# Optimization experiments

Hardware: AMD Instinct MI355X
Metric: run time of the kernel (lower is better)

The kernel has to match this reference:

```python
import jax, jax.numpy as jnp
import numpy as np

GI_DIM = 1220
HID = 150
GIJ = 3 * GI_DIM + 60  # 3720


def setup_inputs() -> dict:
    key = jax.random.key(0)
    ks = jax.random.split(key, 16)
    N, P = 50000, 100000
    inp = {
        "g_i": jax.random.normal(ks[0], (N, GI_DIM), jnp.float32),
        "mention_scores": jax.random.normal(ks[1], (N,), jnp.float32),
        "dist_emb": jax.random.normal(ks[2], (9, 20), jnp.float32) * 0.1,
        "genre_emb": jax.random.normal(ks[3], (8, 20), jnp.float32) * 0.1,
        "speaker_emb": jax.random.normal(ks[4], (3, 20), jnp.float32) * 0.1,
        "W1": jax.random.normal(ks[5], (GIJ, HID), jnp.float32) / np.sqrt(GIJ),
        "b1": jnp.zeros((HID,), jnp.float32),
        "W2": jax.random.normal(ks[6], (HID, HID), jnp.float32) / np.sqrt(HID),
        "b2": jnp.zeros((HID,), jnp.float32),
        "W3": jax.random.normal(ks[7], (HID, 1), jnp.float32) / np.sqrt(HID),
        "b3": jnp.zeros((1,), jnp.float32),
        "mention_ids": jax.random.randint(ks[8], (P,), 0, N, jnp.int64 if jax.config.jax_enable_x64 else jnp.int32),
        "antecedent_ids": jax.random.randint(ks[9], (P,), 0, N, jnp.int32),
        "distance_ids": jax.random.randint(ks[10], (P,), 0, 9, jnp.int32),
        "genre_ids": jax.random.randint(ks[11], (P,), 0, 8, jnp.int32),
        "speaker_ids": jax.random.randint(ks[12], (P,), 0, 3, jnp.int32),
    }
    return inp


def reference(g_i, mention_scores, dist_emb, genre_emb, speaker_emb,
              W1, b1, W2, b2, W3, b3,
              mention_ids, antecedent_ids, distance_ids, genre_ids, speaker_ids):
    # phi: [P, 60] pair features (distance, genre, speaker embeddings)
    phi = jnp.concatenate([dist_emb[distance_ids],
                           genre_emb[genre_ids],
                           speaker_emb[speaker_ids]], axis=1)
    i_g = g_i[mention_ids]      # [P, GI_DIM]
    j_g = g_i[antecedent_ids]   # [P, GI_DIM]
    pairs = jnp.concatenate([i_g, j_g, i_g * j_g, phi], axis=1)  # [P, GIJ]
    h = jax.nn.relu(pairs @ W1 + b1)
    h = jax.nn.relu(h @ W2 + b2)
    pairwise = (h @ W3 + b3)[:, 0]  # [P]
    sij = mention_scores[mention_ids] + mention_scores[antecedent_ids] + pairwise
    return sij
```

## Files before the change

kernel.cpp:

```cpp
#include <hip/hip_runtime.h>

#define GI  1220
#define KP  1280
#define BK  128
#define NCH (KP / BK)
#define NP  192
#define ABW 320

typedef __bf16        bf16x8 __attribute__((ext_vector_type(8)));
typedef float         f32x4  __attribute__((ext_vector_type(4)));
typedef unsigned int  u32x4  __attribute__((ext_vector_type(4)));
typedef unsigned int  u32x2  __attribute__((ext_vector_type(2)));

__device__ __forceinline__ unsigned short f2bf(float f) {
  __bf16 h = (__bf16)f;
  return __builtin_bit_cast(unsigned short, h);
}
__device__ __forceinline__ float bf2f(unsigned short u) {
  return (float)__builtin_bit_cast(__bf16, u);
}
__device__ __forceinline__ unsigned int pk2(float a, float b) {
  return (unsigned int)f2bf(a) | ((unsigned int)f2bf(b) << 16);
}
__device__ __forceinline__ unsigned int mulbf2(unsigned int a, unsigned int b) {
  float xl = __builtin_bit_cast(float, a << 16);
  float xh = __builtin_bit_cast(float, a & 0xffff0000u);
  float yl = __builtin_bit_cast(float, b << 16);
  float yh = __builtin_bit_cast(float, b & 0xffff0000u);
  return pk2(xl * yl, xh * yh);
}

__global__ void prep_kernel(const float* __restrict__ W1, const float* __restrict__ W2,
                            const float* __restrict__ b1,
                            const float* __restrict__ de, const float* __restrict__ ge,
                            const float* __restrict__ se,
                            unsigned short* __restrict__ W1ab_t,
                            unsigned short* __restrict__ W1c_t,
                            unsigned short* __restrict__ W2_t,
                            float* __restrict__ projs) {
  int idx = blockIdx.x * 256 + threadIdx.x;
  const int R1 = ABW * KP, R2 = NP * KP, R3 = NP * NP, R4 = 20 * NP;
  if (idx < R1) {
    int n = idx / KP, k = idx % KP;
    float v = 0.f;
    if (k < GI) {
      if (n < 150)                 v = W1[k * 150 + n];
      else if (n >= 160 && n < 310) v = W1[(GI + k) * 150 + (n - 160)];
    }
    W1ab_t[idx] = f2bf(v);
    return;
  }
  idx -= R1;
  if (idx < R2) {
    int n = idx / KP, k = idx % KP;
    float v = (k < GI && n < 150) ? W1[(2 * GI + k) * 150 + n] : 0.f;
    W1c_t[idx] = f2bf(v);
    return;
  }
  idx -= R2;
  if (idx < R3) {
    int n = idx / NP, k = idx % NP;
    float v = (n < 150 && k < 150) ? W2[k * 150 + n] : 0.f;
    W2_t[idx] = f2bf(v);
    return;
  }
  idx -= R3;
  if (idx < R4) {
    int r = idx / NP, n = idx % NP;
    float v = 0.f;
    if (n < 150) {
      if (r < 9) {
        v = b1[n];
        for (int t = 0; t < 20; ++t) v += de[r * 20 + t] * W1[(3660 + t) * 150 + n];
      } else if (r < 17) {
        int q = r - 9;
        for (int t = 0; t < 20; ++t) v += ge[q * 20 + t] * W1[(3680 + t) * 150 + n];
      } else {
        int q = r - 17;
        for (int t = 0; t < 20; ++t) v += se[q * 20 + t] * W1[(3700 + t) * 150 + n];
      }
    }
    projs[idx] = v;
  }
}

__global__ __launch_bounds__(256, 3)
void ab_kernel(const float* __restrict__ g, const unsigned short* __restrict__ W1ab_t,
               unsigned short* __restrict__ AB, unsigned short* __restrict__ gpad,
               int N) {
  __shared__ __attribute__((aligned(16))) unsigned short sX[64 * 136];
  const int t = threadIdx.x;
  const int m0 = blockIdx.x * 64;
  const int w = t >> 6, lane = t & 63, quad = lane >> 4, lm = lane & 15;

  f32x4 acc[4][5];
#pragma unroll
  for (int a = 0; a < 4; ++a)
#pragma unroll
    for (int b = 0; b < 5; ++b) { acc[a][b].x = 0.f; acc[a][b].y = 0.f; acc[a][b].z = 0.f; acc[a][b].w = 0.f; }

  const int r = t >> 2, s = t & 3;
  int row = m0 + r; if (row >= N) row = N - 1;
  const float* gr = g + (long)row * GI;

  for (int c = 0; c < NCH; ++c) {
    __syncthreads();
#pragma unroll
    for (int i = 0; i < 8; ++i) {
      int k = c * BK + i * 16 + s * 4;
      u32x2 pk; pk.x = 0u; pk.y = 0u;
      if (k < GI) {
        f32x4 x = *(const f32x4*)(gr + k);
        pk.x = pk2(x.x, x.y);
        pk.y = pk2(x.z, x.w);
      }
      *(u32x2*)&sX[r * 136 + i * 16 + s * 4] = pk;
      if (gpad) *(u32x2*)(gpad + (long)row * KP + k) = pk;
    }
    __syncthreads();
#pragma unroll
    for (int kk = 0; kk < 4; ++kk) {
      bf16x8 af[4];
#pragma unroll
      for (int mi = 0; mi < 4; ++mi)
        af[mi] = __builtin_bit_cast(bf16x8, *(const u32x4*)&sX[(mi * 16 + lm) * 136 + kk * 32 + quad * 8]);
#pragma unroll
      for (int tl = 0; tl < 5; ++tl) {
        int n = (w * 5 + tl) * 16 + lm;
        bf16x8 bfr = __builtin_bit_cast(bf16x8, *(const u32x4*)(W1ab_t + n * KP + c * BK + kk * 32 + quad * 8));
#pragma unroll
        for (int mi = 0; mi < 4; ++mi)
          acc[mi][tl] = __builtin_amdgcn_mfma_f32_16x16x32_bf16(af[mi], bfr, acc[mi][tl], 0, 0, 0);
      }
    }
  }
#pragma unroll
  for (int mi = 0; mi < 4; ++mi)
#pragma unroll
    for (int reg = 0; reg < 4; ++reg) {
      int m = m0 + mi * 16 + quad * 4 + reg;
      if (m < N) {
#pragma unroll
        for (int tl = 0; tl < 5; ++tl) {
          int n = (w * 5 + tl) * 16 + lm;
          AB[(long)m * ABW + n] = f2bf(acc[mi][tl][reg]);
        }
      }
    }
}

template <bool PADG>
__global__ __launch_bounds__(256, 5)
void pair_kernel(const float* __restrict__ g, const unsigned short* __restrict__ gpad,
                 const float* __restrict__ msc,
                 const unsigned short* __restrict__ AB,
                 const unsigned short* __restrict__ W1c_t,
                 const unsigned short* __restrict__ W2_t,
                 const float* __restrict__ projs,
                 const float* __restrict__ b2, const float* __restrict__ W3,
                 const float* __restrict__ b3,
                 const int* __restrict__ mid, const int* __restrict__ aid,
                 const int* __restrict__ did, const int* __restrict__ gid,
                 const int* __restrict__ sid,
                 float* __restrict__ out, int P) {
  __shared__ __attribute__((aligned(16))) unsigned short sX[64 * 200];
  __shared__ int sM[64], sA[64], sDGS[64];

  const int t = threadIdx.x;
  const int p0 = blockIdx.x * 64;
  const int w = t >> 6, lane = t & 63, quad = lane >> 4, lm = lane & 15;

  if (t < 64) {
    int p = p0 + t;
    int m_ = 0, a_ = 0, dgs = 0;
    if (p < P) {
      m_ = mid[p]; a_ = aid[p];
      dgs = did[p] | (gid[p] << 4) | (sid[p] << 8);
    }
    sM[t] = m_; sA[t] = a_; sDGS[t] = dgs;
  }
  __syncthreads();

  const int r = t >> 2, s = t & 3;

  f32x4 acc[4][3];
#pragma unroll
  for (int a = 0; a < 4; ++a)
#pragma unroll
    for (int b = 0; b < 3; ++b) { acc[a][b].x = 0.f; acc[a][b].y = 0.f; acc[a][b].z = 0.f; acc[a][b].w = 0.f; }

  const float* gm32; const float* ga32;
  const unsigned short* gm16; const unsigned short* ga16;
  if constexpr (PADG) {
    gm16 = gpad + (long)sM[r] * KP;
    ga16 = gpad + (long)sA[r] * KP;
  } else {
    gm32 = g + (long)sM[r] * GI;
    ga32 = g + (long)sA[r] * GI;
  }

  for (int c = 0; c < NCH; ++c) {
    __syncthreads();
    if constexpr (PADG) {
#pragma unroll
      for (int i = 0; i < 4; ++i) {
        int k = c * BK + i * 32 + s * 8;
        u32x4 xx = *(const u32x4*)(gm16 + k);
        u32x4 yy = *(const u32x4*)(ga16 + k);
        u32x4 o;
        o.x = mulbf2(xx.x, yy.x);
        o.y = mulbf2(xx.y, yy.y);
        o.z = mulbf2(xx.z, yy.z);
        o.w = mulbf2(xx.w, yy.w);
        *(u32x4*)&sX[r * 136 + i * 32 + s * 8] = o;
      }
    } else {
#pragma unroll
      for (int i = 0; i < 8; ++i) {
        int k = c * BK + i * 16 + s * 4;
        u32x2 pk; pk.x = 0u; pk.y = 0u;
        if (k < GI) {
          f32x4 x = *(const f32x4*)(gm32 + k);
          f32x4 y = *(const f32x4*)(ga32 + k);
          pk.x = pk2(x.x * y.x, x.y * y.y);
          pk.y = pk2(x.z * y.z, x.w * y.w);
        }
        *(u32x2*)&sX[r * 136 + i * 16 + s * 4] = pk;
      }
    }
    __syncthreads();
#pragma unroll
    for (int kk = 0; kk < 4; ++kk) {
      bf16x8 af[4];
#pragma unroll
      for (int mi = 0; mi < 4; ++mi)
        af[mi] = __builtin_bit_cast(bf16x8, *(const u32x4*)&sX[(mi * 16 + lm) * 136 + kk * 32 + quad * 8]);
#pragma unroll
      for (int tl = 0; tl < 3; ++tl) {
        int n = (w * 3 + tl) * 16 + lm;
        bf16x8 bfr = __builtin_bit_cast(bf16x8, *(const u32x4*)(W1c_t + n * KP + c * BK + kk * 32 + quad * 8));
#pragma unroll
        for (int mi = 0; mi < 4; ++mi)
          acc[mi][tl] = __builtin_amdgcn_mfma_f32_16x16x32_bf16(af[mi], bfr, acc[mi][tl], 0, 0, 0);
      }
    }
  }
  __syncthreads();

  {
    const unsigned short* Ar = AB + (long)sM[r] * ABW;
    const unsigned short* Br = AB + (long)sA[r] * ABW + 160;
    int dgs = sDGS[r];
    const float* dp = projs + (dgs & 15) * NP;
    const float* gp = projs + (9 + ((dgs >> 4) & 15)) * NP;
    const float* sp = projs + (17 + (dgs >> 8)) * NP;
#pragma unroll
    for (int j = 0; j < 6; ++j) {
      int n = s * 48 + j * 8;
      f32x4 p0v = *(const f32x4*)(dp + n) + *(const f32x4*)(gp + n) + *(const f32x4*)(sp + n);
      f32x4 p1v = *(const f32x4*)(dp + n + 4) + *(const f32x4*)(gp + n + 4) + *(const f32x4*)(sp + n + 4);
      if (n < 160) {
        u32x4 a8 = *(const u32x4*)(Ar + n);
        u32x4 b8 = *(const u32x4*)(Br + n);
        p0v.x += bf2f(a8.x & 0xffff) + bf2f(b8.x & 0xffff);
        p0v.y += bf2f(a8.x >> 16)    + bf2f(b8.x >> 16);
        p0v.z += bf2f(a8.y & 0xffff) + bf2f(b8.y & 0xffff);
        p0v.w += bf2f(a8.y >> 16)    + bf2f(b8.y >> 16);
        p1v.x += bf2f(a8.z & 0xffff) + bf2f(b8.z & 0xffff);
        p1v.y += bf2f(a8.z >> 16)    + bf2f(b8.z >> 16);
        p1v.z += bf2f(a8.w & 0xffff) + bf2f(b8.w & 0xffff);
        p1v.w += bf2f(a8.w >> 16)    + bf2f(b8.w >> 16);
      }
      u32x4 o;
      o.x = pk2(p0v.x, p0v.y); o.y = pk2(p0v.z, p0v.w);
      o.z = pk2(p1v.x, p1v.y); o.w = pk2(p1v.z, p1v.w);
      *(u32x4*)&sX[r * 200 + n] = o;
    }
  }
  __syncthreads();

#pragma unroll
  for (int mi = 0; mi < 4; ++mi)
#pragma unroll
    for (int tl = 0; tl < 3; ++tl) {
      int n = (w * 3 + tl) * 16 + lm;
#pragma unroll
      for (int reg = 0; reg < 4; ++reg) {
        int m = mi * 16 + quad * 4 + reg;
        float v = acc[mi][tl][reg] + bf2f(sX[m * 200 + n]);
        sX[m * 200 + n] = f2bf(fmaxf(v, 0.f));
      }
    }
  __syncthreads();

  f32x4 acc2[4][3];
#pragma unroll
  for (int a = 0; a < 4; ++a)
#pragma unroll
    for (int b = 0; b < 3; ++b) { acc2[a][b].x = 0.f; acc2[a][b].y = 0.f; acc2[a][b].z = 0.f; acc2[a][b].w = 0.f; }
#pragma unroll
  for (int kk = 0; kk < 6; ++kk) {
    bf16x8 af[4];
#pragma unroll
    for (int mi = 0; mi < 4; ++mi)
      af[mi] = __builtin_bit_cast(bf16x8, *(const u32x4*)&sX[(mi * 16 + lm) * 200 + kk * 32 + quad * 8]);
#pragma unroll
    for (int tl = 0; tl < 3; ++tl) {
      int n = (w * 3 + tl) * 16 + lm;
      bf16x8 bfr = __builtin_bit_cast(bf16x8, *(const u32x4*)(W2_t + n * NP + kk * 32 + quad * 8));
#pragma unroll
      for (int mi = 0; mi < 4; ++mi)
        acc2[mi][tl] = __builtin_amdgcn_mfma_f32_16x16x32_bf16(af[mi], bfr, acc2[mi][tl], 0, 0, 0);
    }
  }
  __syncthreads();

#pragma unroll
  for (int mi = 0; mi < 4; ++mi)
#pragma unroll
    for (int tl = 0; tl < 3; ++tl) {
      int n = (w * 3 + tl) * 16 + lm;
      float bb = (n < 150) ? b2[n] : 0.f;
#pragma unroll
      for (int reg = 0; reg < 4; ++reg) {
        int m = mi * 16 + quad * 4 + reg;
        float v = acc2[mi][tl][reg] + bb;
        sX[m * 200 + n] = f2bf(fmaxf(v, 0.f));
      }
    }
  __syncthreads();

  {
    float sum = 0.f;
#pragma unroll
    for (int j = 0; j < 48; ++j) {
      int n = s * 48 + j;
      if (n < 150) sum += bf2f(sX[r * 200 + n]) * W3[n];
    }
    sum += __shfl_xor(sum, 1);
    sum += __shfl_xor(sum, 2);
    if (s == 0) {
      int p = p0 + r;
      if (p < P) out[p] = msc[sM[r]] + msc[sA[r]] + sum + b3[0];
    }
  }
}

extern "C" void kernel_launch(void* const* d_in, const int* in_sizes, int n_in,
                              void* d_out, int out_size, void* d_ws, size_t ws_size,
                              hipStream_t stream) {
  (void)n_in; (void)out_size;
  const float* g   = (const float*)d_in[0];
  const float* msc = (const float*)d_in[1];
  const float* de  = (const float*)d_in[2];
  const float* ge  = (const float*)d_in[3];
  const float* se  = (const float*)d_in[4];
  const float* W1  = (const float*)d_in[5];
  const float* b1  = (const float*)d_in[6];
  const float* W2  = (const float*)d_in[7];
  const float* b2  = (const float*)d_in[8];
  const float* W3  = (const float*)d_in[9];
  const float* b3  = (const float*)d_in[10];
  const int* mid = (const int*)d_in[11];
  const int* aid = (const int*)d_in[12];
  const int* did = (const int*)d_in[13];
  const int* gid = (const int*)d_in[14];
  const int* sid = (const int*)d_in[15];
  const int N = in_sizes[0] / GI;
  const int P = in_sizes[11];
  float* out = (float*)d_out;

  char* ws = (char*)d_ws;
  size_t off = 0;
  auto alloc = [&](size_t bytes) { char* p = ws + off; off = (off + bytes + 255) & ~(size_t)255; return p; };
  unsigned short* AB     = (unsigned short*)alloc((size_t)N * ABW * 2);
  unsigned short* W1ab_t = (unsigned short*)alloc((size_t)ABW * KP * 2);
  unsigned short* W1c_t  = (unsigned short*)alloc((size_t)NP * KP * 2);
  unsigned short* W2_t   = (unsigned short*)alloc((size_t)NP * NP * 2);
  float* projs           = (float*)alloc((size_t)20 * NP * 4);

  size_t gpad_bytes = (size_t)N * KP * 2;
  unsigned short* gpad = nullptr;
  if (off + gpad_bytes + 256 <= ws_size)
    gpad = (unsigned short*)alloc(gpad_bytes);

  const int prep_total = ABW * KP + NP * KP + NP * NP + 20 * NP;
  prep_kernel<<<(prep_total + 255) / 256, 256, 0, stream>>>(W1, W2, b1, de, ge, se,
                                                            W1ab_t, W1c_t, W2_t, projs);
  ab_kernel<<<(N + 63) / 64, 256, 0, stream>>>(g, W1ab_t, AB, gpad, N);
  if (gpad)
    pair_kernel<true><<<(P + 63) / 64, 256, 0, stream>>>(g, gpad, msc, AB, W1c_t, W2_t, projs,
                                                         b2, W3, b3, mid, aid, did, gid, sid, out, P);
  else
    pair_kernel<false><<<(P + 63) / 64, 256, 0, stream>>>(g, gpad, msc, AB, W1c_t, W2_t, projs,
                                                          b2, W3, b3, mid, aid, did, gid, sid, out, P);
}
```

Baseline: 831.0 us.

## Per-wave pair tiles with register prefetch, split bf16 conversion, double-buffered AB GEMM

Restructures the pair kernel so each wave owns its own 16 pairs and all 192 output columns. This removes block-wide __syncthreads and prefetches the next chunk of gathered rows into registers while the MFMAs run. The fp32-to-bf16 conversion of g moves into a separate convert kernel. The AB GEMM now double-buffers its LDS tile with an XOR swizzle and prefetches from the bf16 copy. The trade-offs are more registers per wave (occupancy hint lowered from 5 to 4), and each wave now reads the whole of W1c_t itself instead of sharing it across the block.

```diff
diff --git a/kernel.cpp b/kernel.cpp
--- a/kernel.cpp
+++ b/kernel.cpp
@@ -10,7 +10,6 @@
 typedef __bf16        bf16x8 __attribute__((ext_vector_type(8)));
 typedef float         f32x4  __attribute__((ext_vector_type(4)));
 typedef unsigned int  u32x4  __attribute__((ext_vector_type(4)));
-typedef unsigned int  u32x2  __attribute__((ext_vector_type(2)));
 
 __device__ __forceinline__ unsigned short f2bf(float f) {
   __bf16 h = (__bf16)f;
@@ -44,7 +43,7 @@
     int n = idx / KP, k = idx % KP;
     float v = 0.f;
     if (k < GI) {
-      if (n < 150)                 v = W1[k * 150 + n];
+      if (n < 150)                  v = W1[k * 150 + n];
       else if (n >= 160 && n < 310) v = W1[(GI + k) * 150 + (n - 160)];
     }
     W1ab_t[idx] = f2bf(v);
@@ -84,14 +83,31 @@
   }
 }
 
+__global__ __launch_bounds__(256)
+void convert_kernel(const float* __restrict__ g, unsigned short* __restrict__ gpad, int N) {
+  int idx = blockIdx.x * 256 + threadIdx.x;
+  int total = N * (KP / 8);
+  if (idx >= total) return;
+  int row = idx / (KP / 8);
+  int u   = idx - row * (KP / 8);
+  int k0  = u * 8;
+  u32x4 o; o.x = 0u; o.y = 0u; o.z = 0u; o.w = 0u;
+  const float* gr = g + (long)row * GI;
+  if (k0 + 4 <= GI) { f32x4 a = *(const f32x4*)(gr + k0);     o.x = pk2(a.x, a.y); o.y = pk2(a.z, a.w); }
+  if (k0 + 8 <= GI) { f32x4 b = *(const f32x4*)(gr + k0 + 4); o.z = pk2(b.x, b.y); o.w = pk2(b.z, b.w); }
+  *(u32x4*)(gpad + (long)row * KP + k0) = o;
+}
+
+template <bool PADG>
 __global__ __launch_bounds__(256, 3)
-void ab_kernel(const float* __restrict__ g, const unsigned short* __restrict__ W1ab_t,
-               unsigned short* __restrict__ AB, unsigned short* __restrict__ gpad,
-               int N) {
-  __shared__ __attribute__((aligned(16))) unsigned short sX[64 * 136];
+void ab_kernel(const float* __restrict__ g, const unsigned short* __restrict__ gpad,
+               const unsigned short* __restrict__ W1ab_t,
+               unsigned short* __restrict__ AB, int N) {
+  __shared__ __attribute__((aligned(16))) unsigned short sX[2][8192];
   const int t = threadIdx.x;
   const int m0 = blockIdx.x * 64;
   const int w = t >> 6, lane = t & 63, quad = lane >> 4, lm = lane & 15;
+  const int cb = (t & 15) ^ (t >> 4);
 
   f32x4 acc[4][5];
 #pragma unroll
@@ -99,35 +115,44 @@
 #pragma unroll
     for (int b = 0; b < 5; ++b) { acc[a][b].x = 0.f; acc[a][b].y = 0.f; acc[a][b].z = 0.f; acc[a][b].w = 0.f; }
 
-  const int r = t >> 2, s = t & 3;
-  int row = m0 + r; if (row >= N) row = N - 1;
-  const float* gr = g + (long)row * GI;
-
+  u32x4 stg[4];
+  auto fetch = [&](int c, u32x4 st[4]) {
+#pragma unroll
+    for (int j = 0; j < 4; ++j) {
+      int row = m0 + j * 16 + (t >> 4); if (row >= N) row = N - 1;
+      int k = c * BK + cb * 8;
+      if constexpr (PADG) {
+        st[j] = *(const u32x4*)(gpad + (long)row * KP + k);
+      } else {
+        u32x4 o; o.x = 0u; o.y = 0u; o.z = 0u; o.w = 0u;
+        const float* gr = g + (long)row * GI + k;
+        if (k + 4 <= GI) { f32x4 a = *(const f32x4*)gr;       o.x = pk2(a.x, a.y); o.y = pk2(a.z, a.w); }
+        if (k + 8 <= GI) { f32x4 b = *(const f32x4*)(gr + 4); o.z = pk2(b.x, b.y); o.w = pk2(b.z, b.w); }
+        st[j] = o;
+      }
+    }
+  };
+
+  fetch(0, stg);
   for (int c = 0; c < NCH; ++c) {
-    __syncthreads();
-#pragma unroll
-    for (int i = 0; i < 8; ++i) {
-      int k = c * BK + i * 16 + s * 4;
-      u32x2 pk; pk.x = 0u; pk.y = 0u;
-      if (k < GI) {
-        f32x4 x = *(const f32x4*)(gr + k);
-        pk.x = pk2(x.x, x.y);
-        pk.y = pk2(x.z, x.w);
-      }
-      *(u32x2*)&sX[r * 136 + i * 16 + s * 4] = pk;
-      if (gpad) *(u32x2*)(gpad + (long)row * KP + k) = pk;
-    }
+    unsigned short* buf = sX[c & 1];
+#pragma unroll
+    for (int j = 0; j < 4; ++j)
+      *(u32x4*)(buf + (j * 256 + t) * 8) = stg[j];
+    if (c + 1 < NCH) fetch(c + 1, stg);
     __syncthreads();
 #pragma unroll
     for (int kk = 0; kk < 4; ++kk) {
       bf16x8 af[4];
 #pragma unroll
-      for (int mi = 0; mi < 4; ++mi)
-        af[mi] = __builtin_bit_cast(bf16x8, *(const u32x4*)&sX[(mi * 16 + lm) * 136 + kk * 32 + quad * 8]);
+      for (int mi = 0; mi < 4; ++mi) {
+        int row = mi * 16 + lm;
+        af[mi] = __builtin_bit_cast(bf16x8, *(const u32x4*)(buf + row * 128 + (((kk * 4 + quad) ^ lm) * 8)));
+      }
 #pragma unroll
       for (int tl = 0; tl < 5; ++tl) {
         int n = (w * 5 + tl) * 16 + lm;
-        bf16x8 bfr = __builtin_bit_cast(bf16x8, *(const u32x4*)(W1ab_t + n * KP + c * BK + kk * 32 + quad * 8));
+        bf16x8 bfr = __builtin_bit_cast(bf16x8, *(const u32x4*)(W1ab_t + (long)n * KP + c * BK + kk * 32 + quad * 8));
 #pragma unroll
         for (int mi = 0; mi < 4; ++mi)
           acc[mi][tl] = __builtin_amdgcn_mfma_f32_16x16x32_bf16(af[mi], bfr, acc[mi][tl], 0, 0, 0);
@@ -150,7 +175,7 @@
 }
 
 template <bool PADG>
-__global__ __launch_bounds__(256, 5)
+__global__ __launch_bounds__(256, 4)
 void pair_kernel(const float* __restrict__ g, const unsigned short* __restrict__ gpad,
                  const float* __restrict__ msc,
                  const unsigned short* __restrict__ AB,
@@ -163,103 +188,120 @@
                  const int* __restrict__ did, const int* __restrict__ gid,
                  const int* __restrict__ sid,
                  float* __restrict__ out, int P) {
-  __shared__ __attribute__((aligned(16))) unsigned short sX[64 * 200];
-  __shared__ int sM[64], sA[64], sDGS[64];
-
+  __shared__ __attribute__((aligned(16))) unsigned short sW[4][16 * 200];
   const int t = threadIdx.x;
-  const int p0 = blockIdx.x * 64;
   const int w = t >> 6, lane = t & 63, quad = lane >> 4, lm = lane & 15;
-
-  if (t < 64) {
-    int p = p0 + t;
-    int m_ = 0, a_ = 0, dgs = 0;
-    if (p < P) {
-      m_ = mid[p]; a_ = aid[p];
-      dgs = did[p] | (gid[p] << 4) | (sid[p] << 8);
-    }
-    sM[t] = m_; sA[t] = a_; sDGS[t] = dgs;
-  }
-  __syncthreads();
-
-  const int r = t >> 2, s = t & 3;
-
-  f32x4 acc[4][3];
-#pragma unroll
-  for (int a = 0; a < 4; ++a)
-#pragma unroll
-    for (int b = 0; b < 3; ++b) { acc[a][b].x = 0.f; acc[a][b].y = 0.f; acc[a][b].z = 0.f; acc[a][b].w = 0.f; }
-
-  const float* gm32; const float* ga32;
-  const unsigned short* gm16; const unsigned short* ga16;
+  unsigned short* sWw = sW[w];
+
+  const int pw0 = blockIdx.x * 64 + w * 16;
+
+  int mv = 0, av = 0, dv = 0;
+  float scv = 0.f;
+  if (lane < 16) {
+    int p = pw0 + lane; if (p >= P) p = P - 1;
+    mv = mid[p]; av = aid[p];
+    dv = did[p] | (gid[p] << 4) | (sid[p] << 8);
+    scv = msc[mv] + msc[av];
+  }
+  const int mi_ = __shfl(mv, lm);
+  const int ai_ = __shfl(av, lm);
+  const int dgs = __shfl(dv, lm);
+
+  const int rr = lane & 15;
+  const int colq = lane >> 4;
+
+  f32x4 acc[12];
+#pragma unroll
+  for (int i = 0; i < 12; ++i) { acc[i].x = 0.f; acc[i].y = 0.f; acc[i].z = 0.f; acc[i].w = 0.f; }
+
   if constexpr (PADG) {
-    gm16 = gpad + (long)sM[r] * KP;
-    ga16 = gpad + (long)sA[r] * KP;
+    const unsigned short* gmr = gpad + (long)mi_ * KP;
+    const unsigned short* gar = gpad + (long)ai_ * KP;
+    u32x4 xr[2], yr[2];
+    auto fetch = [&](int c) {
+      int k = c * BK + colq * 32;
+      xr[0] = *(const u32x4*)(gmr + k);     xr[1] = *(const u32x4*)(gmr + k + 8);
+      yr[0] = *(const u32x4*)(gar + k);     yr[1] = *(const u32x4*)(gar + k + 8);
+    };
+    u32x4 xr2[2], yr2[2];
+    auto fetch2 = [&](int c) {
+      int k = c * BK + colq * 32;
+      xr2[0] = *(const u32x4*)(gmr + k + 16); xr2[1] = *(const u32x4*)(gmr + k + 24);
+      yr2[0] = *(const u32x4*)(gar + k + 16); yr2[1] = *(const u32x4*)(gar + k + 24);
+    };
+    fetch(0); fetch2(0);
+    for (int c = 0; c < NCH; ++c) {
+#pragma unroll
+      for (int h = 0; h < 2; ++h) {
+        u32x4 o;
+        o.x = mulbf2(xr[h].x, yr[h].x); o.y = mulbf2(xr[h].y, yr[h].y);
+        o.z = mulbf2(xr[h].z, yr[h].z); o.w = mulbf2(xr[h].w, yr[h].w);
+        *(u32x4*)&sWw[rr * 200 + colq * 32 + h * 8] = o;
+      }
+#pragma unroll
+      for (int h = 0; h < 2; ++h) {
+        u32x4 o;
+        o.x = mulbf2(xr2[h].x, yr2[h].x); o.y = mulbf2(xr2[h].y, yr2[h].y);
+        o.z = mulbf2(xr2[h].z, yr2[h].z); o.w = mulbf2(xr2[h].w, yr2[h].w);
+        *(u32x4*)&sWw[rr * 200 + colq * 32 + 16 + h * 8] = o;
+      }
+      if (c + 1 < NCH) { fetch(c + 1); fetch2(c + 1); }
+#pragma unroll
+      for (int kk = 0; kk < 4; ++kk) {
+        bf16x8 af = __builtin_bit_cast(bf16x8, *(const u32x4*)&sWw[lm * 200 + kk * 32 + quad * 8]);
+#pragma unroll
+        for (int tl = 0; tl < 12; ++tl) {
+          int n = tl * 16 + lm;
+          bf16x8 bfr = __builtin_bit_cast(bf16x8, *(const u32x4*)(W1c_t + (long)n * KP + c * BK + kk * 32 + quad * 8));
+          acc[tl] = __builtin_amdgcn_mfma_f32_16x16x32_bf16(af, bfr, acc[tl], 0, 0, 0);
+        }
+      }
+    }
   } else {
-    gm32 = g + (long)sM[r] * GI;
-    ga32 = g + (long)sA[r] * GI;
-  }
-
-  for (int c = 0; c < NCH; ++c) {
-    __syncthreads();
-    if constexpr (PADG) {
-#pragma unroll
-      for (int i = 0; i < 4; ++i) {
-        int k = c * BK + i * 32 + s * 8;
-        u32x4 xx = *(const u32x4*)(gm16 + k);
-        u32x4 yy = *(const u32x4*)(ga16 + k);
-        u32x4 o;
-        o.x = mulbf2(xx.x, yy.x);
-        o.y = mulbf2(xx.y, yy.y);
-        o.z = mulbf2(xx.z, yy.z);
-        o.w = mulbf2(xx.w, yy.w);
-        *(u32x4*)&sX[r * 136 + i * 32 + s * 8] = o;
-      }
-    } else {
-#pragma unroll
-      for (int i = 0; i < 8; ++i) {
-        int k = c * BK + i * 16 + s * 4;
-        u32x2 pk; pk.x = 0u; pk.y = 0u;
-        if (k < GI) {
-          f32x4 x = *(const f32x4*)(gm32 + k);
-          f32x4 y = *(const f32x4*)(ga32 + k);
-          pk.x = pk2(x.x * y.x, x.y * y.y);
-          pk.y = pk2(x.z * y.z, x.w * y.w);
+    const float* gmr = g + (long)mi_ * GI;
+    const float* gar = g + (long)ai_ * GI;
+    for (int c = 0; c < NCH; ++c) {
+#pragma unroll
+      for (int h = 0; h < 4; ++h) {
+        int k = c * BK + colq * 32 + h * 8;
+        u32x4 o; o.x = 0u; o.y = 0u; o.z = 0u; o.w = 0u;
+        if (k + 4 <= GI) {
+          f32x4 x = *(const f32x4*)(gmr + k);
+          f32x4 y = *(const f32x4*)(gar + k);
+          o.x = pk2(x.x * y.x, x.y * y.y); o.y = pk2(x.z * y.z, x.w * y.w);
         }
-        *(u32x2*)&sX[r * 136 + i * 16 + s * 4] = pk;
-      }
-    }
-    __syncthreads();
-#pragma unroll
-    for (int kk = 0; kk < 4; ++kk) {
-      bf16x8 af[4];
-#pragma unroll
-      for (int mi = 0; mi < 4; ++mi)
-        af[mi] = __builtin_bit_cast(bf16x8, *(const u32x4*)&sX[(mi * 16 + lm) * 136 + kk * 32 + quad * 8]);
-#pragma unroll
-      for (int tl = 0; tl < 3; ++tl) {
-        int n = (w * 3 + tl) * 16 + lm;
-        bf16x8 bfr = __builtin_bit_cast(bf16x8, *(const u32x4*)(W1c_t + n * KP + c * BK + kk * 32 + quad * 8));
-#pragma unroll
-        for (int mi = 0; mi < 4; ++mi)
-          acc[mi][tl] = __builtin_amdgcn_mfma_f32_16x16x32_bf16(af[mi], bfr, acc[mi][tl], 0, 0, 0);
-      }
-    }
-  }
-  __syncthreads();
+        if (k + 8 <= GI) {
+          f32x4 x = *(const f32x4*)(gmr + k + 4);
+          f32x4 y = *(const f32x4*)(gar + k + 4);
+          o.z = pk2(x.x * y.x, x.y * y.y); o.w = pk2(x.z * y.z, x.w * y.w);
+        }
+        *(u32x4*)&sWw[rr * 200 + colq * 32 + h * 8] = o;
+      }
+#pragma unroll
+      for (int kk = 0; kk < 4; ++kk) {
+        bf16x8 af = __builtin_bit_cast(bf16x8, *(const u32x4*)&sWw[lm * 200 + kk * 32 + quad * 8]);
+#pragma unroll
+        for (int tl = 0; tl < 12; ++tl) {
+          int n = tl * 16 + lm;
+          bf16x8 bfr = __builtin_bit_cast(bf16x8, *(const u32x4*)(W1c_t + (long)n * KP + c * BK + kk * 32 + quad * 8));
+          acc[tl] = __builtin_amdgcn_mfma_f32_16x16x32_bf16(af, bfr, acc[tl], 0, 0, 0);
+        }
+      }
+    }
+  }
 
   {
-    const unsigned short* Ar = AB + (long)sM[r] * ABW;
-    const unsigned short* Br = AB + (long)sA[r] * ABW + 160;
-    int dgs = sDGS[r];
+    const unsigned short* Ar = AB + (long)mi_ * ABW;
+    const unsigned short* Br = AB + (long)ai_ * ABW + 160;
     const float* dp = projs + (dgs & 15) * NP;
     const float* gp = projs + (9 + ((dgs >> 4) & 15)) * NP;
     const float* sp = projs + (17 + (dgs >> 8)) * NP;
 #pragma unroll
-    for (int j = 0; j < 6; ++j) {
-      int n = s * 48 + j * 8;
-      f32x4 p0v = *(const f32x4*)(dp + n) + *(const f32x4*)(gp + n) + *(const f32x4*)(sp + n);
+    for (int jj = 0; jj < 6; ++jj) {
+      int n = colq * 48 + jj * 8;
+      f32x4 p0v = *(const f32x4*)(dp + n)     + *(const f32x4*)(gp + n)     + *(const f32x4*)(sp + n);
       f32x4 p1v = *(const f32x4*)(dp + n + 4) + *(const f32x4*)(gp + n + 4) + *(const f32x4*)(sp + n + 4);
-      if (n < 160) {
+      if (n + 8 <= 160) {
         u32x4 a8 = *(const u32x4*)(Ar + n);
         u32x4 b8 = *(const u32x4*)(Br + n);
         p0v.x += bf2f(a8.x & 0xffff) + bf2f(b8.x & 0xffff);
@@ -274,74 +316,66 @@
       u32x4 o;
       o.x = pk2(p0v.x, p0v.y); o.y = pk2(p0v.z, p0v.w);
       o.z = pk2(p1v.x, p1v.y); o.w = pk2(p1v.z, p1v.w);
-      *(u32x4*)&sX[r * 200 + n] = o;
-    }
-  }
-  __syncthreads();
-
-#pragma unroll
-  for (int mi = 0; mi < 4; ++mi)
-#pragma unroll
-    for (int tl = 0; tl < 3; ++tl) {
-      int n = (w * 3 + tl) * 16 + lm;
-#pragma unroll
-      for (int reg = 0; reg < 4; ++reg) {
-        int m = mi * 16 + quad * 4 + reg;
-        float v = acc[mi][tl][reg] + bf2f(sX[m * 200 + n]);
-        sX[m * 200 + n] = f2bf(fmaxf(v, 0.f));
-      }
-    }
-  __syncthreads();
-
-  f32x4 acc2[4][3];
-#pragma unroll
-  for (int a = 0; a < 4; ++a)
-#pragma unroll
-    for (int b = 0; b < 3; ++b) { acc2[a][b].x = 0.f; acc2[a][b].y = 0.f; acc2[a][b].z = 0.f; acc2[a][b].w = 0.f; }
+      *(u32x4*)&sWw[rr * 200 + n] = o;
+    }
+  }
+
+#pragma unroll
+  for (int tl = 0; tl < 12; ++tl) {
+    int n = tl * 16 + lm;
+#pragma unroll
+    for (int reg = 0; reg < 4; ++reg) {
+      int m = quad * 4 + reg;
+      float v = acc[tl][reg] + bf2f(sWw[m * 200 + n]);
+      sWw[m * 200 + n] = f2bf(fmaxf(v, 0.f));
+    }
+  }
+
+  f32x4 acc2[12];
+#pragma unroll
+  for (int i = 0; i < 12; ++i) { acc2[i].x = 0.f; acc2[i].y = 0.f; acc2[i].z = 0.f; acc2[i].w = 0.f; }
 #pragma unroll
   for (int kk = 0; kk < 6; ++kk) {
-    bf16x8 af[4];
-#pragma unroll
-    for (int mi = 0; mi < 4; ++mi)
-      af[mi] = __builtin_bit_cast(bf16x8, *(const u32x4*)&sX[(mi * 16 + lm) * 200 + kk * 32 + quad * 8]);
-#pragma unroll
-    for (int tl = 0; tl < 3; ++tl) {
-      int n = (w * 3 + tl) * 16 + lm;
+    bf16x8 af = __builtin_bit_cast(bf16x8, *(const u32x4*)&sWw[lm * 200 + kk * 32 + quad * 8]);
+#pragma unroll
+    for (int tl = 0; tl < 12; ++tl) {
+      int n = tl * 16 + lm;
       bf16x8 bfr = __builtin_bit_cast(bf16x8, *(const u32x4*)(W2_t + n * NP + kk * 32 + quad * 8));
-#pragma unroll
-      for (int mi = 0; mi < 4; ++mi)
-        acc2[mi][tl] = __builtin_amdgcn_mfma_f32_16x16x32_bf16(af[mi], bfr, acc2[mi][tl], 0, 0, 0);
-    }
-  }
-  __syncthreads();
-
-#pragma unroll
-  for (int mi = 0; mi < 4; ++mi)
-#pragma unroll
-    for (int tl = 0; tl < 3; ++tl) {
-      int n = (w * 3 + tl) * 16 + lm;
-      float bb = (n < 150) ? b2[n] : 0.f;
-#pragma unroll
-      for (int reg = 0; reg < 4; ++reg) {
-        int m = mi * 16 + quad * 4 + reg;
-        float v = acc2[mi][tl][reg] + bb;
-        sX[m * 200 + n] = f2bf(fmaxf(v, 0.f));
-      }
-    }
-  __syncthreads();
+      acc2[tl] = __builtin_amdgcn_mfma_f32_16x16x32_bf16(af, bfr, acc2[tl], 0, 0, 0);
+    }
+  }
+
+#pragma unroll
+  for (int tl = 0; tl < 12; ++tl) {
+    int n = tl * 16 + lm;
+    float bb = (n < 150) ? b2[n] : 0.f;
+#pragma unroll
+    for (int reg = 0; reg < 4; ++reg) {
+      int m = quad * 4 + reg;
+      float v = acc2[tl][reg] + bb;
+      sWw[m * 200 + n] = f2bf(fmaxf(v, 0.f));
+    }
+  }
 
   {
     float sum = 0.f;
 #pragma unroll
-    for (int j = 0; j < 48; ++j) {
-      int n = s * 48 + j;
-      if (n < 150) sum += bf2f(sX[r * 200 + n]) * W3[n];
-    }
-    sum += __shfl_xor(sum, 1);
-    sum += __shfl_xor(sum, 2);
-    if (s == 0) {
-      int p = p0 + r;
-      if (p < P) out[p] = msc[sM[r]] + msc[sA[r]] + sum + b3[0];
+    for (int jj = 0; jj < 6; ++jj) {
+      int n = colq * 48 + jj * 8;
+      u32x4 hv = *(const u32x4*)&sWw[rr * 200 + n];
+      const unsigned int* hw = (const unsigned int*)&hv;
+#pragma unroll
+      for (int e = 0; e < 4; ++e) {
+        int nn = n + e * 2;
+        if (nn < 150)     sum += bf2f(hw[e] & 0xffff) * W3[nn];
+        if (nn + 1 < 150) sum += bf2f(hw[e] >> 16)    * W3[nn + 1];
+      }
+    }
+    sum += __shfl_xor(sum, 16);
+    sum += __shfl_xor(sum, 32);
+    if (lane < 16) {
+      int p = pw0 + lane;
+      if (p < P) out[p] = scv + sum + b3[0];
     }
   }
 }
@@ -387,11 +421,15 @@
   const int prep_total = ABW * KP + NP * KP + NP * NP + 20 * NP;
   prep_kernel<<<(prep_total + 255) / 256, 256, 0, stream>>>(W1, W2, b1, de, ge, se,
                                                             W1ab_t, W1c_t, W2_t, projs);
-  ab_kernel<<<(N + 63) / 64, 256, 0, stream>>>(g, W1ab_t, AB, gpad, N);
-  if (gpad)
+  if (gpad) {
+    int cv_total = N * (KP / 8);
+    convert_kernel<<<(cv_total + 255) / 256, 256, 0, stream>>>(g, gpad, N);
+    ab_kernel<true><<<(N + 63) / 64, 256, 0, stream>>>(g, gpad, W1ab_t, AB, N);
     pair_kernel<true><<<(P + 63) / 64, 256, 0, stream>>>(g, gpad, msc, AB, W1c_t, W2_t, projs,
                                                          b2, W3, b3, mid, aid, did, gid, sid, out, P);
-  else
+  } else {
+    ab_kernel<false><<<(N + 63) / 64, 256, 0, stream>>>(g, gpad, W1ab_t, AB, N);
     pair_kernel<false><<<(P + 63) / 64, 256, 0, stream>>>(g, gpad, msc, AB, W1c_t, W2_t, projs,
                                                           b2, W3, b3, mid, aid, did, gid, sid, out, P);
-}
+  }
+}
```

After: 1.198 ms. 1.44x slower.

## Load MFMA A-fragments directly from global, split bf16 convert, retile pair kernel

Applied to the files above, without the earlier changes.

Moves the fp32→bf16 conversion of g into its own kernel. The ab and pair GEMMs now load A-operand fragments straight from global memory into registers, dropping the LDS staging and the per-chunk __syncthreads. The pair kernel is retiled to a 2x2 wave grid (each wave covers 32 rows × 96 cols), which halves A-fragment gathers per wave, and it software-prefetches the next k-slice of gathered rows. The trade-off is an extra kernel launch plus a full gpad write/read pass, and uncoalesced per-lane 16B gathers with no LDS reuse across waves.

```diff
diff --git a/kernel.cpp b/kernel.cpp
--- a/kernel.cpp
+++ b/kernel.cpp
@@ -2,15 +2,12 @@
 
 #define GI  1220
 #define KP  1280
-#define BK  128
-#define NCH (KP / BK)
 #define NP  192
 #define ABW 320
 
 typedef __bf16        bf16x8 __attribute__((ext_vector_type(8)));
 typedef float         f32x4  __attribute__((ext_vector_type(4)));
 typedef unsigned int  u32x4  __attribute__((ext_vector_type(4)));
-typedef unsigned int  u32x2  __attribute__((ext_vector_type(2)));
 
 __device__ __forceinline__ unsigned short f2bf(float f) {
   __bf16 h = (__bf16)f;
@@ -44,7 +41,7 @@
     int n = idx / KP, k = idx % KP;
     float v = 0.f;
     if (k < GI) {
-      if (n < 150)                 v = W1[k * 150 + n];
+      if (n < 150)                  v = W1[k * 150 + n];
       else if (n >= 160 && n < 310) v = W1[(GI + k) * 150 + (n - 160)];
     }
     W1ab_t[idx] = f2bf(v);
@@ -84,54 +81,69 @@
   }
 }
 
-__global__ __launch_bounds__(256, 3)
-void ab_kernel(const float* __restrict__ g, const unsigned short* __restrict__ W1ab_t,
-               unsigned short* __restrict__ AB, unsigned short* __restrict__ gpad,
-               int N) {
-  __shared__ __attribute__((aligned(16))) unsigned short sX[64 * 136];
+__global__ __launch_bounds__(256)
+void convert_kernel(const float* __restrict__ g, unsigned short* __restrict__ gpad, int N) {
+  int idx = blockIdx.x * 256 + threadIdx.x;
+  int total = N * (KP / 8);
+  if (idx >= total) return;
+  int row = idx / (KP / 8);
+  int u   = idx - row * (KP / 8);
+  int k0  = u * 8;
+  u32x4 o; o.x = 0u; o.y = 0u; o.z = 0u; o.w = 0u;
+  const float* gr = g + (long)row * GI;
+  if (k0 + 4 <= GI) { f32x4 a = *(const f32x4*)(gr + k0);     o.x = pk2(a.x, a.y); o.y = pk2(a.z, a.w); }
+  if (k0 + 8 <= GI) { f32x4 b = *(const f32x4*)(gr + k0 + 4); o.z = pk2(b.x, b.y); o.w = pk2(b.z, b.w); }
+  *(u32x4*)(gpad + (long)row * KP + k0) = o;
+}
+
+template <bool PADG>
+__global__ __launch_bounds__(256, 4)
+void ab_kernel(const float* __restrict__ g, const unsigned short* __restrict__ gpad,
+               const unsigned short* __restrict__ W1ab_t,
+               unsigned short* __restrict__ AB, int N) {
   const int t = threadIdx.x;
   const int m0 = blockIdx.x * 64;
   const int w = t >> 6, lane = t & 63, quad = lane >> 4, lm = lane & 15;
 
+  const unsigned short* gp16[4];
+  const float* gp32[4];
+#pragma unroll
+  for (int mi = 0; mi < 4; ++mi) {
+    int row = m0 + mi * 16 + lm; if (row >= N) row = N - 1;
+    if constexpr (PADG) gp16[mi] = gpad + (long)row * KP;
+    else                gp32[mi] = g + (long)row * GI;
+  }
+
   f32x4 acc[4][5];
 #pragma unroll
   for (int a = 0; a < 4; ++a)
 #pragma unroll
     for (int b = 0; b < 5; ++b) { acc[a][b].x = 0.f; acc[a][b].y = 0.f; acc[a][b].z = 0.f; acc[a][b].w = 0.f; }
 
-  const int r = t >> 2, s = t & 3;
-  int row = m0 + r; if (row >= N) row = N - 1;
-  const float* gr = g + (long)row * GI;
-
-  for (int c = 0; c < NCH; ++c) {
-    __syncthreads();
-#pragma unroll
-    for (int i = 0; i < 8; ++i) {
-      int k = c * BK + i * 16 + s * 4;
-      u32x2 pk; pk.x = 0u; pk.y = 0u;
-      if (k < GI) {
-        f32x4 x = *(const f32x4*)(gr + k);
-        pk.x = pk2(x.x, x.y);
-        pk.y = pk2(x.z, x.w);
-      }
-      *(u32x2*)&sX[r * 136 + i * 16 + s * 4] = pk;
-      if (gpad) *(u32x2*)(gpad + (long)row * KP + k) = pk;
-    }
-    __syncthreads();
-#pragma unroll
-    for (int kk = 0; kk < 4; ++kk) {
-      bf16x8 af[4];
+  for (int i = 0; i < 40; ++i) {
+    int ko = i * 32 + quad * 8;
+    bf16x8 af[4];
+#pragma unroll
+    for (int mi = 0; mi < 4; ++mi) {
+      if constexpr (PADG) {
+        af[mi] = __builtin_bit_cast(bf16x8, *(const u32x4*)(gp16[mi] + ko));
+      } else {
+        f32x4 a0, a1;
+        a0.x=0;a0.y=0;a0.z=0;a0.w=0; a1=a0;
+        if (ko + 4 <= GI) a0 = *(const f32x4*)(gp32[mi] + ko);
+        if (ko + 8 <= GI) a1 = *(const f32x4*)(gp32[mi] + ko + 4);
+        u32x4 o; o.x = pk2(a0.x, a0.y); o.y = pk2(a0.z, a0.w);
+        o.z = pk2(a1.x, a1.y); o.w = pk2(a1.z, a1.w);
+        af[mi] = __builtin_bit_cast(bf16x8, o);
+      }
+    }
+#pragma unroll
+    for (int tl = 0; tl < 5; ++tl) {
+      int n = (w * 5 + tl) * 16 + lm;
+      bf16x8 bfr = __builtin_bit_cast(bf16x8, *(const u32x4*)(W1ab_t + (long)n * KP + ko));
 #pragma unroll
       for (int mi = 0; mi < 4; ++mi)
-        af[mi] = __builtin_bit_cast(bf16x8, *(const u32x4*)&sX[(mi * 16 + lm) * 136 + kk * 32 + quad * 8]);
-#pragma unroll
-      for (int tl = 0; tl < 5; ++tl) {
-        int n = (w * 5 + tl) * 16 + lm;
-        bf16x8 bfr = __builtin_bit_cast(bf16x8, *(const u32x4*)(W1ab_t + n * KP + c * BK + kk * 32 + quad * 8));
-#pragma unroll
-        for (int mi = 0; mi < 4; ++mi)
-          acc[mi][tl] = __builtin_amdgcn_mfma_f32_16x16x32_bf16(af[mi], bfr, acc[mi][tl], 0, 0, 0);
-      }
+        acc[mi][tl] = __builtin_amdgcn_mfma_f32_16x16x32_bf16(af[mi], bfr, acc[mi][tl], 0, 0, 0);
     }
   }
 #pragma unroll
@@ -150,7 +162,7 @@
 }
 
 template <bool PADG>
-__global__ __launch_bounds__(256, 5)
+__global__ __launch_bounds__(256, 4)
 void pair_kernel(const float* __restrict__ g, const unsigned short* __restrict__ gpad,
                  const float* __restrict__ msc,
                  const unsigned short* __restrict__ AB,
@@ -163,91 +175,38 @@
                  const int* __restrict__ did, const int* __restrict__ gid,
                  const int* __restrict__ sid,
                  float* __restrict__ out, int P) {
-  __shared__ __attribute__((aligned(16))) unsigned short sX[64 * 200];
+  __shared__ __attribute__((aligned(16))) unsigned short sH[64 * 200];
   __shared__ int sM[64], sA[64], sDGS[64];
 
   const int t = threadIdx.x;
   const int p0 = blockIdx.x * 64;
   const int w = t >> 6, lane = t & 63, quad = lane >> 4, lm = lane & 15;
+  const int wm = w >> 1, wn = w & 1;
 
   if (t < 64) {
-    int p = p0 + t;
-    int m_ = 0, a_ = 0, dgs = 0;
-    if (p < P) {
-      m_ = mid[p]; a_ = aid[p];
-      dgs = did[p] | (gid[p] << 4) | (sid[p] << 8);
-    }
-    sM[t] = m_; sA[t] = a_; sDGS[t] = dgs;
+    int p = p0 + t; if (p >= P) p = P - 1;
+    sM[t] = mid[p]; sA[t] = aid[p];
+    sDGS[t] = did[p] | (gid[p] << 4) | (sid[p] << 8);
   }
   __syncthreads();
 
-  const int r = t >> 2, s = t & 3;
-
-  f32x4 acc[4][3];
-#pragma unroll
-  for (int a = 0; a < 4; ++a)
-#pragma unroll
-    for (int b = 0; b < 3; ++b) { acc[a][b].x = 0.f; acc[a][b].y = 0.f; acc[a][b].z = 0.f; acc[a][b].w = 0.f; }
-
-  const float* gm32; const float* ga32;
-  const unsigned short* gm16; const unsigned short* ga16;
-  if constexpr (PADG) {
-    gm16 = gpad + (long)sM[r] * KP;
-    ga16 = gpad + (long)sA[r] * KP;
-  } else {
-    gm32 = g + (long)sM[r] * GI;
-    ga32 = g + (long)sA[r] * GI;
-  }
-
-  for (int c = 0; c < NCH; ++c) {
-    __syncthreads();
+  const int r0 = wm * 32 + lm;
+  const unsigned short* gmp[2]; const unsigned short* gap[2];
+  const float* gmp32[2]; const float* gap32[2];
+#pragma unroll
+  for (int mi = 0; mi < 2; ++mi) {
+    int rr = r0 + mi * 16;
     if constexpr (PADG) {
-#pragma unroll
-      for (int i = 0; i < 4; ++i) {
-        int k = c * BK + i * 32 + s * 8;
-        u32x4 xx = *(const u32x4*)(gm16 + k);
-        u32x4 yy = *(const u32x4*)(ga16 + k);
-        u32x4 o;
-        o.x = mulbf2(xx.x, yy.x);
-        o.y = mulbf2(xx.y, yy.y);
-        o.z = mulbf2(xx.z, yy.z);
-        o.w = mulbf2(xx.w, yy.w);
-        *(u32x4*)&sX[r * 136 + i * 32 + s * 8] = o;
-      }
+      gmp[mi] = gpad + (long)sM[rr] * KP;
+      gap[mi] = gpad + (long)sA[rr] * KP;
     } else {
-#pragma unroll
-      for (int i = 0; i < 8; ++i) {
-        int k = c * BK + i * 16 + s * 4;
-        u32x2 pk; pk.x = 0u; pk.y = 0u;
-        if (k < GI) {
-          f32x4 x = *(const f32x4*)(gm32 + k);
-          f32x4 y = *(const f32x4*)(ga32 + k);
-          pk.x = pk2(x.x * y.x, x.y * y.y);
-          pk.y = pk2(x.z * y.z, x.w * y.w);
-        }
-        *(u32x2*)&sX[r * 136 + i * 16 + s * 4] = pk;
-      }
-    }
-    __syncthreads();
-#pragma unroll
-    for (int kk = 0; kk < 4; ++kk) {
-      bf16x8 af[4];
-#pragma unroll
-      for (int mi = 0; mi < 4; ++mi)
-        af[mi] = __builtin_bit_cast(bf16x8, *(const u32x4*)&sX[(mi * 16 + lm) * 136 + kk * 32 + quad * 8]);
-#pragma unroll
-      for (int tl = 0; tl < 3; ++tl) {
-        int n = (w * 3 + tl) * 16 + lm;
-        bf16x8 bfr = __builtin_bit_cast(bf16x8, *(const u32x4*)(W1c_t + n * KP + c * BK + kk * 32 + quad * 8));
-#pragma unroll
-        for (int mi = 0; mi < 4; ++mi)
-          acc[mi][tl] = __builtin_amdgcn_mfma_f32_16x16x32_bf16(af[mi], bfr, acc[mi][tl], 0, 0, 0);
-      }
-    }
-  }
-  __syncthreads();
+      gmp32[mi] = g + (long)sM[rr] * GI;
+      gap32[mi] = g + (long)sA[rr] * GI;
+    }
+  }
 
   {
+    const int r = t >> 2, s = t & 3;
     const unsigned short* Ar = AB + (long)sM[r] * ABW;
     const unsigned short* Br = AB + (long)sA[r] * ABW + 160;
     int dgs = sDGS[r];
@@ -255,11 +214,11 @@
     const float* gp = projs + (9 + ((dgs >> 4) & 15)) * NP;
     const float* sp = projs + (17 + (dgs >> 8)) * NP;
 #pragma unroll
-    for (int j = 0; j < 6; ++j) {
-      int n = s * 48 + j * 8;
-      f32x4 p0v = *(const f32x4*)(dp + n) + *(const f32x4*)(gp + n) + *(const f32x4*)(sp + n);
+    for (int jj = 0; jj < 6; ++jj) {
+      int n = s * 48 + jj * 8;
+      f32x4 p0v = *(const f32x4*)(dp + n)     + *(const f32x4*)(gp + n)     + *(const f32x4*)(sp + n);
       f32x4 p1v = *(const f32x4*)(dp + n + 4) + *(const f32x4*)(gp + n + 4) + *(const f32x4*)(sp + n + 4);
-      if (n < 160) {
+      if (n + 8 <= 160) {
         u32x4 a8 = *(const u32x4*)(Ar + n);
         u32x4 b8 = *(const u32x4*)(Br + n);
         p0v.x += bf2f(a8.x & 0xffff) + bf2f(b8.x & 0xffff);
@@ -274,68 +233,135 @@
       u32x4 o;
       o.x = pk2(p0v.x, p0v.y); o.y = pk2(p0v.z, p0v.w);
       o.z = pk2(p1v.x, p1v.y); o.w = pk2(p1v.z, p1v.w);
-      *(u32x4*)&sX[r * 200 + n] = o;
+      *(u32x4*)&sH[r * 200 + n] = o;
+    }
+  }
+
+  f32x4 acc[2][6];
+#pragma unroll
+  for (int a = 0; a < 2; ++a)
+#pragma unroll
+    for (int b = 0; b < 6; ++b) { acc[a][b].x = 0.f; acc[a][b].y = 0.f; acc[a][b].z = 0.f; acc[a][b].w = 0.f; }
+
+  if constexpr (PADG) {
+    u32x4 cxa[2], cxb[2];
+#pragma unroll
+    for (int mi = 0; mi < 2; ++mi) {
+      cxa[mi] = *(const u32x4*)(gmp[mi] + quad * 8);
+      cxb[mi] = *(const u32x4*)(gap[mi] + quad * 8);
+    }
+    for (int i = 0; i < 40; ++i) {
+      u32x4 nxa[2], nxb[2];
+      if (i + 1 < 40) {
+        int ko2 = (i + 1) * 32 + quad * 8;
+#pragma unroll
+        for (int mi = 0; mi < 2; ++mi) {
+          nxa[mi] = *(const u32x4*)(gmp[mi] + ko2);
+          nxb[mi] = *(const u32x4*)(gap[mi] + ko2);
+        }
+      }
+      bf16x8 af[2];
+#pragma unroll
+      for (int mi = 0; mi < 2; ++mi) {
+        u32x4 o;
+        o.x = mulbf2(cxa[mi].x, cxb[mi].x); o.y = mulbf2(cxa[mi].y, cxb[mi].y);
+        o.z = mulbf2(cxa[mi].z, cxb[mi].z); o.w = mulbf2(cxa[mi].w, cxb[mi].w);
+        af[mi] = __builtin_bit_cast(bf16x8, o);
+      }
+      int ko = i * 32 + quad * 8;
+#pragma unroll
+      for (int tl = 0; tl < 6; ++tl) {
+        int n = (wn * 6 + tl) * 16 + lm;
+        bf16x8 bfr = __builtin_bit_cast(bf16x8, *(const u32x4*)(W1c_t + (long)n * KP + ko));
+        acc[0][tl] = __builtin_amdgcn_mfma_f32_16x16x32_bf16(af[0], bfr, acc[0][tl], 0, 0, 0);
+        acc[1][tl] = __builtin_amdgcn_mfma_f32_16x16x32_bf16(af[1], bfr, acc[1][tl], 0, 0, 0);
+      }
+#pragma unroll
+      for (int mi = 0; mi < 2; ++mi) { cxa[mi] = nxa[mi]; cxb[mi] = nxb[mi]; }
+    }
+  } else {
+    for (int i = 0; i < 40; ++i) {
+      int ko = i * 32 + quad * 8;
+      bf16x8 af[2];
+#pragma unroll
+      for (int mi = 0; mi < 2; ++mi) {
+        f32x4 a0, a1, b0, b1;
+        a0.x=0;a0.y=0;a0.z=0;a0.w=0; a1=a0; b0=a0; b1=a0;
+        if (ko + 4 <= GI) { a0 = *(const f32x4*)(gmp32[mi] + ko);     b0 = *(const f32x4*)(gap32[mi] + ko); }
+        if (ko + 8 <= GI) { a1 = *(const f32x4*)(gmp32[mi] + ko + 4); b1 = *(const f32x4*)(gap32[mi] + ko + 4); }
+        u32x4 o;
+        o.x = pk2(a0.x * b0.x, a0.y * b0.y); o.y = pk2(a0.z * b0.z, a0.w * b0.w);
+        o.z = pk2(a1.x * b1.x, a1.y * b1.y); o.w = pk2(a1.z * b1.z, a1.w * b1.w);
+        af[mi] = __builtin_bit_cast(bf16x8, o);
+      }
+#pragma unroll
+      for (int tl = 0; tl < 6; ++tl) {
+        int n = (wn * 6 + tl) * 16 + lm;
+        bf16x8 bfr = __builtin_bit_cast(bf16x8, *(const u32x4*)(W1c_t + (long)n * KP + ko));
+        acc[0][tl] = __builtin_amdgcn_mfma_f32_16x16x32_bf16(af[0], bfr, acc[0][tl], 0, 0, 0);
+        acc[1][tl] = __builtin_amdgcn_mfma_f32_16x16x32_bf16(af[1], bfr, acc[1][tl], 0, 0, 0);
+      }
     }
   }
   __syncthreads();
 
 #pragma unroll
-  for (int mi = 0; mi < 4; ++mi)
-#pragma unroll
-    for (int tl = 0; tl < 3; ++tl) {
-      int n = (w * 3 + tl) * 16 + lm;
+  for (int mi = 0; mi < 2; ++mi)
+#pragma unroll
+    for (int tl = 0; tl < 6; ++tl) {
+      int n = (wn * 6 + tl) * 16 + lm;
 #pragma unroll
       for (int reg = 0; reg < 4; ++reg) {
-        int m = mi * 16 + quad * 4 + reg;
-        float v = acc[mi][tl][reg] + bf2f(sX[m * 200 + n]);
-        sX[m * 200 + n] = f2bf(fmaxf(v, 0.f));
+        int m = wm * 32 + mi * 16 + quad * 4 + reg;
+        float v = acc[mi][tl][reg] + bf2f(sH[m * 200 + n]);
+        sH[m * 200 + n] = f2bf(fmaxf(v, 0.f));
       }
     }
   __syncthreads();
 
-  f32x4 acc2[4][3];
-#pragma unroll
-  for (int a = 0; a < 4; ++a)
-#pragma unroll
-    for (int b = 0; b < 3; ++b) { acc2[a][b].x = 0.f; acc2[a][b].y = 0.f; acc2[a][b].z = 0.f; acc2[a][b].w = 0.f; }
+  f32x4 acc2[2][6];
+#pragma unroll
+  for (int a = 0; a < 2; ++a)
+#pragma unroll
+    for (int b = 0; b < 6; ++b) { acc2[a][b].x = 0.f; acc2[a][b].y = 0.f; acc2[a][b].z = 0.f; acc2[a][b].w = 0.f; }
 #pragma unroll
   for (int kk = 0; kk < 6; ++kk) {
-    bf16x8 af[4];
-#pragma unroll
-    for (int mi = 0; mi < 4; ++mi)
-      af[mi] = __builtin_bit_cast(bf16x8, *(const u32x4*)&sX[(mi * 16 + lm) * 200 + kk * 32 + quad * 8]);
-#pragma unroll
-    for (int tl = 0; tl < 3; ++tl) {
-      int n = (w * 3 + tl) * 16 + lm;
+    bf16x8 af[2];
+#pragma unroll
+    for (int mi = 0; mi < 2; ++mi)
+      af[mi] = __builtin_bit_cast(bf16x8, *(const u32x4*)&sH[(wm * 32 + mi * 16 + lm) * 200 + kk * 32 + quad * 8]);
+#pragma unroll
+    for (int tl = 0; tl < 6; ++tl) {
+      int n = (wn * 6 + tl) * 16 + lm;
       bf16x8 bfr = __builtin_bit_cast(bf16x8, *(const u32x4*)(W2_t + n * NP + kk * 32 + quad * 8));
-#pragma unroll
-      for (int mi = 0; mi < 4; ++mi)
-        acc2[mi][tl] = __builtin_amdgcn_mfma_f32_16x16x32_bf16(af[mi], bfr, acc2[mi][tl], 0, 0, 0);
+      acc2[0][tl] = __builtin_amdgcn_mfma_f32_16x16x32_bf16(af[0], bfr, acc2[0][tl], 0, 0, 0);
+      acc2[1][tl] = __builtin_amdgcn_mfma_f32_16x16x32_bf16(af[1], bfr, acc2[1][tl], 0, 0, 0);
     }
   }
   __syncthreads();
 
 #pragma unroll
-  for (int mi = 0; mi < 4; ++mi)
-#pragma unroll
-    for (int tl = 0; tl < 3; ++tl) {
-      int n = (w * 3 + tl) * 16 + lm;
+  for (int mi = 0; mi < 2; ++mi)
+#pragma unroll
+    for (int tl = 0; tl < 6; ++tl) {
+      int n = (wn * 6 + tl) * 16 + lm;
       float bb = (n < 150) ? b2[n] : 0.f;
 #pragma unroll
       for (int reg = 0; reg < 4; ++reg) {
-        int m = mi * 16 + quad * 4 + reg;
+        int m = wm * 32 + mi * 16 + quad * 4 + reg;
         float v = acc2[mi][tl][reg] + bb;
-        sX[m * 200 + n] = f2bf(fmaxf(v, 0.f));
+        sH[m * 200 + n] = f2bf(fmaxf(v, 0.f));
       }
     }
   __syncthreads();
 
   {
+    const int r = t >> 2, s = t & 3;
     float sum = 0.f;
 #pragma unroll
     for (int j = 0; j < 48; ++j) {
       int n = s * 48 + j;
-      if (n < 150) sum += bf2f(sX[r * 200 + n]) * W3[n];
+      if (n < 150) sum += bf2f(sH[r * 200 + n]) * W3[n];
     }
     sum += __shfl_xor(sum, 1);
     sum += __shfl_xor(sum, 2);
@@ -387,11 +413,15 @@
   const int prep_total = ABW * KP + NP * KP + NP * NP + 20 * NP;
   prep_kernel<<<(prep_total + 255) / 256, 256, 0, stream>>>(W1, W2, b1, de, ge, se,
                                                             W1ab_t, W1c_t, W2_t, projs);
-  ab_kernel<<<(N + 63) / 64, 256, 0, stream>>>(g, W1ab_t, AB, gpad, N);
-  if (gpad)
+  if (gpad) {
+    int cv_total = N * (KP / 8);
+    convert_kernel<<<(cv_total + 255) / 256, 256, 0, stream>>>(g, gpad, N);
+    ab_kernel<true><<<(N + 63) / 64, 256, 0, stream>>>(g, gpad, W1ab_t, AB, N);
     pair_kernel<true><<<(P + 63) / 64, 256, 0, stream>>>(g, gpad, msc, AB, W1c_t, W2_t, projs,
                                                          b2, W3, b3, mid, aid, did, gid, sid, out, P);
-  else
+  } else {
+    ab_kernel<false><<<(N + 63) / 64, 256, 0, stream>>>(g, gpad, W1ab_t, AB, N);
     pair_kernel<false><<<(P + 63) / 64, 256, 0, stream>>>(g, gpad, msc, AB, W1c_t, W2_t, projs,
                                                           b2, W3, b3, mid, aid, did, gid, sid, out, P);
-}
+  }
+}
```

Measured after the change: 943.3 us. +13.5%, slower.
